# Kernel tuning notes

Measured on AMD Instinct MI355X. Metric: run time of the kernel, lower is better.

## Reference

```python
import jax, jax.numpy as jnp
import numpy as np

NUM_HEADS = 12
SCRA_SCALING = 10.0
EPS = 1e-12  # F.normalize default eps


def setup_inputs() -> dict:
    key = jax.random.key(0)
    ks = jax.random.split(key, 5)
    B, N, C = 2, 2048, 768
    return {
        "x": jax.random.normal(ks[0], (B, N, C), dtype=jnp.float32),
        "qkv_w": jax.random.normal(ks[1], (3 * C, C), dtype=jnp.float32) * 0.02,
        "qkv_b": jax.random.normal(ks[2], (3 * C,), dtype=jnp.float32) * 0.02,
        "proj_w": jax.random.normal(ks[3], (C, C), dtype=jnp.float32) * 0.02,
        "proj_b": jax.random.normal(ks[4], (C,), dtype=jnp.float32) * 0.02,
    }


def reference(x, qkv_w, qkv_b, proj_w, proj_b):
    B, N, C = x.shape
    H = NUM_HEADS
    D = C // H
    scale = D ** -0.5

    xt = jnp.transpose(x, (1, 0, 2))  # [N, B, C]
    qkv = xt @ qkv_w.T + qkv_b        # [N, B, 3C]
    q, k, v = jnp.split(qkv, 3, axis=-1)

    def to_bh(t):  # [N, B, C] -> [B*H, N, D]
        return jnp.transpose(t.reshape(N, B * H, D), (1, 0, 2))

    q, k, v = to_bh(q), to_bh(k), to_bh(v)

    # Stage 1: standard attention
    attn = jax.nn.softmax(jnp.einsum('bnd,bmd->bnm', q, k) * scale, axis=-1)
    out = jnp.einsum('bnm,bmd->bnd', attn, v)  # [B*H, N, D]
    out = jnp.transpose(out, (1, 0, 2)).reshape(N, B, C)
    out = out @ proj_w.T + proj_b              # first proj
    out = jnp.transpose(out.reshape(N, B * H, D), (1, 0, 2))  # [B*H, N, D]

    # Stage 2: self-correlation attention with data-dependent masking
    norm = jnp.linalg.norm(out, axis=-1, keepdims=True)
    sim_tokens = out / jnp.maximum(norm, EPS)
    sim = jnp.einsum('bnd,bmd->bnm', sim_tokens, sim_tokens) * SCRA_SCALING
    sim = jnp.where(sim < 0, -jnp.inf, sim)
    sim = jax.nn.softmax(sim, axis=-1)
    out2 = jnp.einsum('bnm,bmd->bnd', sim, v)
    out2 = jnp.transpose(out2, (1, 0, 2)).reshape(N, B, C)
    out2 = out2 @ proj_w.T + proj_b            # second proj (same weights)

    return jnp.transpose(out2, (1, 0, 2))      # [B, N, C]
```

## Files before the change

kernel.cpp:

```cpp
#include <hip/hip_runtime.h>

typedef unsigned short u16;
typedef __bf16 bf16_t;
typedef bf16_t bf16x8 __attribute__((ext_vector_type(8)));
typedef float f32x4 __attribute__((ext_vector_type(4)));

static __device__ __forceinline__ u16 f2bf(float f) {
  unsigned u = __builtin_bit_cast(unsigned, f);
  u += 0x7FFFu + ((u >> 16) & 1u);
  return (u16)(u >> 16);
}
static __device__ __forceinline__ bf16x8 ldfrag(const u16* p) {
  return __builtin_bit_cast(bf16x8, *(const uint4*)p);
}
static __device__ __forceinline__ float fexp2(float x) {
#if __has_builtin(__builtin_amdgcn_exp2f)
  return __builtin_amdgcn_exp2f(x);
#else
  return __expf(x * 0.69314718056f);
#endif
}
static __device__ __forceinline__ unsigned pack_hi16(unsigned hi, unsigned lo) {
#if __has_builtin(__builtin_amdgcn_perm)
  return __builtin_amdgcn_perm(hi, lo, 0x07060302u);
#else
  return (lo >> 16) | (hi & 0xFFFF0000u);
#endif
}
static __device__ __forceinline__ int sw(int row, int chunk) {
  return (row << 6) + ((chunk ^ (row & 7)) << 3);
}

#define XSZ 3145728
#define QWSZ 1769472
#define PWSZ 589824

__global__ __launch_bounds__(256) void convert_all(
    const float* __restrict__ x, const float* __restrict__ qw,
    const float* __restrict__ pw, u16* __restrict__ xb,
    u16* __restrict__ qwb, u16* __restrict__ pwb)
{
  const int i = (blockIdx.x * 256 + threadIdx.x) * 8;
  const float* src; u16* dst; int off;
  if (i < XSZ) { src = x; dst = xb; off = i; }
  else if (i < XSZ + QWSZ) { src = qw; dst = qwb; off = i - XSZ; }
  else { src = pw; dst = pwb; off = i - (XSZ + QWSZ); }
  float4 a = *(const float4*)(src + off), b = *(const float4*)(src + off + 4);
  u16 t[8] = {f2bf(a.x), f2bf(a.y), f2bf(a.z), f2bf(a.w),
              f2bf(b.x), f2bf(b.y), f2bf(b.z), f2bf(b.w)};
  *(uint4*)(dst + off) = *(const uint4*)t;
}

template<int MODE>
__global__ __launch_bounds__(256, 3) void gemm_nt(
    const u16* __restrict__ A, const u16* __restrict__ W,
    const float* __restrict__ bias,
    u16* __restrict__ d0, u16* __restrict__ d1, u16* __restrict__ d2,
    float* __restrict__ df)
{
  __shared__ __align__(16) u16 sA[2][64 * 64];
  __shared__ __align__(16) u16 sB[2][128 * 64];
  const int tid = threadIdx.x;
  const int m0 = blockIdx.y * 64, n0 = blockIdx.x * 128;
  const int w = tid >> 6, lane = tid & 63, l16 = lane & 15, quad = lane >> 4;
  const int wm = (w >> 1) * 32, wn = (w & 1) * 64;

  f32x4 acc[2][4] = {};
  const int sr = tid >> 3, ch = tid & 7, sc = ch * 8;

  #pragma unroll
  for (int p = 0; p < 2; p++)
    *(uint4*)(sA[0] + sw(sr + p * 32, ch)) =
        *(const uint4*)(A + (size_t)(m0 + sr + p * 32) * 768 + sc);
  #pragma unroll
  for (int p = 0; p < 4; p++)
    *(uint4*)(sB[0] + sw(sr + p * 32, ch)) =
        *(const uint4*)(W + (size_t)(n0 + sr + p * 32) * 768 + sc);
  __syncthreads();

  for (int kt = 0; kt < 12; kt++) {
    const int buf = kt & 1;
    const bool pre = (kt + 1 < 12);
    uint4 rab[2], rb[4];
    if (pre) {
      const int kc = (kt + 1) * 64 + sc;
      #pragma unroll
      for (int p = 0; p < 2; p++)
        rab[p] = *(const uint4*)(A + (size_t)(m0 + sr + p * 32) * 768 + kc);
      #pragma unroll
      for (int p = 0; p < 4; p++)
        rb[p] = *(const uint4*)(W + (size_t)(n0 + sr + p * 32) * 768 + kc);
    }
    #pragma unroll
    for (int ks = 0; ks < 2; ks++) {
      bf16x8 af[2], bfv[4];
      #pragma unroll
      for (int i = 0; i < 2; i++)
        af[i] = ldfrag(sA[buf] + sw(wm + i * 16 + l16, ks * 4 + quad));
      #pragma unroll
      for (int i = 0; i < 4; i++)
        bfv[i] = ldfrag(sB[buf] + sw(wn + i * 16 + l16, ks * 4 + quad));
      #pragma unroll
      for (int mi = 0; mi < 2; mi++)
        #pragma unroll
        for (int ni = 0; ni < 4; ni++)
          acc[mi][ni] = __builtin_amdgcn_mfma_f32_16x16x32_bf16(af[mi], bfv[ni], acc[mi][ni], 0, 0, 0);
    }
    if (pre) {
      #pragma unroll
      for (int p = 0; p < 2; p++)
        *(uint4*)(sA[buf ^ 1] + sw(sr + p * 32, ch)) = rab[p];
      #pragma unroll
      for (int p = 0; p < 4; p++)
        *(uint4*)(sB[buf ^ 1] + sw(sr + p * 32, ch)) = rb[p];
    }
    __syncthreads();
  }

  if (MODE == 0) {
    #pragma unroll
    for (int ni = 0; ni < 4; ni++) {
      const int gn = n0 + wn + ni * 16 + l16;
      const float bv = bias[gn];
      const int which = gn / 768;
      const int c = gn - which * 768, hh = c >> 6, d = c & 63;
      #pragma unroll
      for (int mi = 0; mi < 2; mi++) {
        const int gm0 = m0 + wm + mi * 16 + quad * 4;
        const int bb = gm0 >> 11, nt0 = gm0 & 2047;
        if (which == 2) {
          u16 t[4];
          #pragma unroll
          for (int r = 0; r < 4; r++) t[r] = f2bf(acc[mi][ni][r] + bv);
          *(uint2*)(d2 + (((size_t)(bb * 12 + hh)) * 64 + d) * 2048 + nt0) =
              *(const uint2*)t;
        } else {
          u16* dst = (which == 0) ? d0 : d1;
          #pragma unroll
          for (int r = 0; r < 4; r++)
            dst[(((size_t)(bb * 12 + hh)) * 2048 + nt0 + r) * 64 + d] =
                f2bf(acc[mi][ni][r] + bv);
        }
      }
    }
  } else if (MODE == 1) {
    #pragma unroll
    for (int mi = 0; mi < 2; mi++) {
      #pragma unroll
      for (int r = 0; r < 4; r++) {
        float v[4]; float ss = 0.f;
        #pragma unroll
        for (int ni = 0; ni < 4; ni++) {
          v[ni] = acc[mi][ni][r] + bias[n0 + wn + ni * 16 + l16];
          ss += v[ni] * v[ni];
        }
        #pragma unroll
        for (int off = 1; off < 16; off <<= 1) ss += __shfl_xor(ss, off);
        const float scl = 1.f / fmaxf(sqrtf(ss), 1e-12f);
        const int gm = m0 + wm + mi * 16 + quad * 4 + r;
        const int nt = gm >> 1, b = gm & 1;
        #pragma unroll
        for (int ni = 0; ni < 4; ni++) {
          const int gn = n0 + wn + ni * 16 + l16, h = gn >> 6, d = gn & 63;
          d0[(((size_t)(b * 12 + h)) * 2048 + nt) * 64 + d] = f2bf(v[ni] * scl);
        }
      }
    }
  } else {
    #pragma unroll
    for (int ni = 0; ni < 4; ni++) {
      const int gn = n0 + wn + ni * 16 + l16;
      const float bv = bias[gn];
      #pragma unroll
      for (int mi = 0; mi < 2; mi++) {
        #pragma unroll
        for (int r = 0; r < 4; r++) {
          const int gm = m0 + wm + mi * 16 + quad * 4 + r;
          const int nt = gm >> 1, b = gm & 1;
          df[((size_t)b * 2048 + nt) * 768 + gn] = acc[mi][ni][r] + bv;
        }
      }
    }
  }
}

template<int MODE>
__global__ __launch_bounds__(256, 2) void flash_attn(
    const u16* __restrict__ Qm, const u16* __restrict__ Km,
    const u16* __restrict__ VT,
    float* __restrict__ partN, float* __restrict__ partL)
{
  constexpr int N = 2048;
  __shared__ __align__(16) u16 sU[128 * 64];
  __shared__ __align__(16) u16 sK[64 * 64];
  __shared__ __align__(16) u16 sVT[64 * 64];
  const int tid = threadIdx.x;
  const int bh = blockIdx.y;
  const int qt = blockIdx.x >> 1, half = blockIdx.x & 1;
  const int m0 = qt * 128, j0 = half * 1024;
  const int w = tid >> 6, lane = tid & 63, l16 = lane & 15, quad = lane >> 4;

  constexpr float SC = (MODE == 1) ? 0.18033688011112042f
                                   : 14.426950408889634f;
  constexpr float M0 = (MODE == 1) ? 24.f : 14.6f;

  const u16* kbase = Km + (size_t)bh * N * 64;
  const u16* vbase = VT + (size_t)bh * 64 * N;
  const int qr = tid >> 1, qc = (tid & 1) * 4;
  const int sr4 = tid >> 2, c4 = tid & 3;
  {
    const u16* qp = Qm + ((size_t)bh * N + m0 + qr) * 64 + qc * 8;
    #pragma unroll
    for (int j = 0; j < 4; j++)
      *(uint4*)(sU + sw(qr, qc + j)) = *(const uint4*)(qp + j * 8);
    const u16* kp = kbase + (size_t)(j0 + sr4) * 64;
    *(uint4*)(sK + sw(sr4, c4))     = *(const uint4*)(kp + c4 * 8);
    *(uint4*)(sK + sw(sr4, c4 + 4)) = *(const uint4*)(kp + c4 * 8 + 32);
    const u16* vp = vbase + (size_t)sr4 * N + j0;
    *(uint4*)(sVT + sw(sr4, c4))     = *(const uint4*)(vp + c4 * 8);
    *(uint4*)(sVT + sw(sr4, c4 + 4)) = *(const uint4*)(vp + c4 * 8 + 32);
  }
  __syncthreads();
  bf16x8 qf[2][2];
  #pragma unroll
  for (int qg = 0; qg < 2; qg++) {
    qf[qg][0] = ldfrag(sU + sw(w * 32 + qg * 16 + l16, quad));
    qf[qg][1] = ldfrag(sU + sw(w * 32 + qg * 16 + l16, quad + 4));
  }
  asm volatile("s_waitcnt lgkmcnt(0)" ::: "memory");

  bf16x8 ones;
  #pragma unroll
  for (int i = 0; i < 8; i++) ones[i] = (bf16_t)1.0f;

  f32x4 oacc[2][4] = {};
  f32x4 lacc[2] = {};

  for (int it = 0; it < 16; it++) {
    uint4 pk0, pk1, pv0, pv1;
    const bool pre = (it + 1 < 16);
    if (pre) {
      const int j1 = j0 + (it + 1) * 64;
      const u16* kp = kbase + (size_t)(j1 + sr4) * 64;
      pk0 = *(const uint4*)(kp + c4 * 8);
      pk1 = *(const uint4*)(kp + c4 * 8 + 32);
      const u16* vp = vbase + (size_t)sr4 * N + j1;
      pv0 = *(const uint4*)(vp + c4 * 8);
      pv1 = *(const uint4*)(vp + c4 * 8 + 32);
    }

    f32x4 s[2][4];
    #pragma unroll
    for (int jt = 0; jt < 4; jt++) {
      bf16x8 kf0 = ldfrag(sK + sw(jt * 16 + l16, quad));
      bf16x8 kf1 = ldfrag(sK + sw(jt * 16 + l16, quad + 4));
      #pragma unroll
      for (int qg = 0; qg < 2; qg++) {
        f32x4 a = {};
        a = __builtin_amdgcn_mfma_f32_16x16x32_bf16(kf0, qf[qg][0], a, 0, 0, 0);
        a = __builtin_amdgcn_mfma_f32_16x16x32_bf16(kf1, qf[qg][1], a, 0, 0, 0);
        s[qg][jt] = a;
      }
    }

    #pragma unroll
    for (int qg = 0; qg < 2; qg++) {
      const int prow = w * 32 + qg * 16 + l16;
      #pragma unroll
      for (int jt = 0; jt < 4; jt++) {
        unsigned pu[4];
        #pragma unroll
        for (int r = 0; r < 4; r++) {
          const float a = s[qg][jt][r];
          float p = fexp2(fmaf(a, SC, -M0));
          if (MODE == 2 && a < 0.f) p = 0.f;
          pu[r] = __builtin_bit_cast(unsigned, p) & 0xFFFF0000u;
        }
        uint2 pkk;
        pkk.x = pack_hi16(pu[1], pu[0]);
        pkk.y = pack_hi16(pu[3], pu[2]);
        *(uint2*)(sU + sw(prow, 2 * jt + (quad >> 1)) + (quad & 1) * 4) = pkk;
      }
    }

    asm volatile("s_waitcnt lgkmcnt(0)" ::: "memory");
    bf16x8 pf[2][2];
    #pragma unroll
    for (int qg = 0; qg < 2; qg++) {
      pf[qg][0] = ldfrag(sU + sw(w * 32 + qg * 16 + l16, quad));
      pf[qg][1] = ldfrag(sU + sw(w * 32 + qg * 16 + l16, quad + 4));
    }

    #pragma unroll
    for (int d4 = 0; d4 < 4; d4++) {
      bf16x8 v0 = ldfrag(sVT + sw(d4 * 16 + l16, quad));
      bf16x8 v1 = ldfrag(sVT + sw(d4 * 16 + l16, quad + 4));
      #pragma unroll
      for (int qg = 0; qg < 2; qg++) {
        oacc[qg][d4] = __builtin_amdgcn_mfma_f32_16x16x32_bf16(v0, pf[qg][0], oacc[qg][d4], 0, 0, 0);
        oacc[qg][d4] = __builtin_amdgcn_mfma_f32_16x16x32_bf16(v1, pf[qg][1], oacc[qg][d4], 0, 0, 0);
      }
    }
    #pragma unroll
    for (int qg = 0; qg < 2; qg++) {
      lacc[qg] = __builtin_amdgcn_mfma_f32_16x16x32_bf16(ones, pf[qg][0], lacc[qg], 0, 0, 0);
      lacc[qg] = __builtin_amdgcn_mfma_f32_16x16x32_bf16(ones, pf[qg][1], lacc[qg], 0, 0, 0);
    }

    __syncthreads();
    if (pre) {
      *(uint4*)(sK + sw(sr4, c4))      = pk0;
      *(uint4*)(sK + sw(sr4, c4 + 4))  = pk1;
      *(uint4*)(sVT + sw(sr4, c4))     = pv0;
      *(uint4*)(sVT + sw(sr4, c4 + 4)) = pv1;
    }
    __syncthreads();
  }

  const int blk = bh * 32 + blockIdx.x;
  float* pN = partN + (size_t)blk * 8192 + tid * 32;
  #pragma unroll
  for (int qg = 0; qg < 2; qg++) {
    #pragma unroll
    for (int d4 = 0; d4 < 4; d4++)
      *(f32x4*)(pN + qg * 16 + d4 * 4) = oacc[qg][d4];
    if (quad == 0)
      partL[blk * 128 + w * 32 + qg * 16 + l16] = lacc[qg][0];
  }
}

__global__ __launch_bounds__(256) void combine_flash(
    const float* __restrict__ partN, const float* __restrict__ partL,
    u16* __restrict__ Ob)
{
  const int pair = blockIdx.x;
  const int bh = pair >> 4, qt = pair & 15;
  const int b = bh / 12, h = bh % 12;
  const int m0 = qt * 128;
  const int tid = threadIdx.x;
  const int w = tid >> 6, lane = tid & 63, l16 = lane & 15, quad = lane >> 4;
  const int blk0 = bh * 32 + qt * 2, blk1 = blk0 + 1;
  const float* n0 = partN + (size_t)blk0 * 8192 + tid * 32;
  const float* n1 = partN + (size_t)blk1 * 8192 + tid * 32;
  #pragma unroll
  for (int qg = 0; qg < 2; qg++) {
    const int qrow = w * 32 + qg * 16 + l16;
    const float l0 = partL[blk0 * 128 + qrow];
    const float l1 = partL[blk1 * 128 + qrow];
    const float inv = 1.f / fmaxf(l0 + l1, 1e-30f);
    const int query = m0 + qrow;
    u16* obase = Ob + ((size_t)query * 2 + b) * 768 + h * 64;
    #pragma unroll
    for (int d4 = 0; d4 < 4; d4++) {
      float4 a = *(const float4*)(n0 + qg * 16 + d4 * 4);
      float4 c = *(const float4*)(n1 + qg * 16 + d4 * 4);
      u16 t[4] = {f2bf((a.x + c.x) * inv), f2bf((a.y + c.y) * inv),
                  f2bf((a.z + c.z) * inv), f2bf((a.w + c.w) * inv)};
      *(uint2*)(obase + d4 * 16 + quad * 4) = *(const uint2*)t;
    }
  }
}

extern "C" void kernel_launch(void* const* d_in, const int* in_sizes, int n_in,
                              void* d_out, int out_size, void* d_ws, size_t ws_size,
                              hipStream_t stream) {
  const float* x      = (const float*)d_in[0];
  const float* qkv_w  = (const float*)d_in[1];
  const float* qkv_b  = (const float*)d_in[2];
  const float* proj_w = (const float*)d_in[3];
  const float* proj_b = (const float*)d_in[4];
  float* out = (float*)d_out;

  const size_t SZ = (size_t)24 * 2048 * 64;
  char* ws = (char*)d_ws;
  u16* vtb = (u16*)ws;
  size_t off = SZ * 2;
  u16* qwb = (u16*)(ws + off); off += (size_t)QWSZ * 2;
  u16* pwb = (u16*)(ws + off); off += (size_t)PWSZ * 2;
  u16* qb  = (u16*)(ws + off); off += SZ * 2;
  u16* kb  = (u16*)(ws + off); off += SZ * 2;
  float* partN = (float*)(ws + off); off += (size_t)768 * 8192 * 4;
  float* partL = (float*)(ws + off); off += (size_t)768 * 128 * 4;
  u16* xb = (u16*)partN;
  u16* o1 = qb;
  u16* o2 = qb;
  u16* st = kb;

  convert_all<<<2688, 256, 0, stream>>>(x, qkv_w, proj_w, xb, qwb, pwb);
  gemm_nt<0><<<dim3(18, 64), 256, 0, stream>>>(xb, qwb, qkv_b, qb, kb, vtb, nullptr);
  flash_attn<1><<<dim3(32, 24), 256, 0, stream>>>(qb, kb, vtb, partN, partL);
  combine_flash<<<384, 256, 0, stream>>>(partN, partL, o1);
  gemm_nt<1><<<dim3(6, 64), 256, 0, stream>>>(o1, pwb, proj_b, st, nullptr, nullptr, nullptr);
  flash_attn<2><<<dim3(32, 24), 256, 0, stream>>>(st, st, vtb, partN, partL);
  combine_flash<<<384, 256, 0, stream>>>(partN, partL, o2);
  gemm_nt<2><<<dim3(6, 64), 256, 0, stream>>>(o2, pwb, proj_b, nullptr, nullptr, nullptr, out);
}
```

Before: 231.9 us.

## Enlarge flash query tile to 256, split keys four ways, double-buffer K/V

The flash attention kernel now processes 256 query rows per block (64 per wave) and splits the key range into four 512-key chunks, so each K/V tile loaded into shared memory is reused across twice as many queries. K/V tiles are double-buffered in LDS, which removes one of the two block barriers per iteration, and the score-to-probability conversion is fused into the QK loop so the score array is no longer held. The combine kernel now sums four partials per query tile, and the workspace is rearranged so the qkv weight copy sits inside the enlarged partial buffer. In exchange, register pressure rises (twice as many accumulators per wave), LDS use grows, and the partial buffers written and read back are twice as large.

```diff
diff --git a/kernel.cpp b/kernel.cpp
--- a/kernel.cpp
+++ b/kernel.cpp
@@ -191,13 +191,13 @@
     float* __restrict__ partN, float* __restrict__ partL)
 {
   constexpr int N = 2048;
-  __shared__ __align__(16) u16 sU[128 * 64];
-  __shared__ __align__(16) u16 sK[64 * 64];
-  __shared__ __align__(16) u16 sVT[64 * 64];
+  __shared__ __align__(16) u16 sU[256 * 64];
+  __shared__ __align__(16) u16 sK[2][64 * 64];
+  __shared__ __align__(16) u16 sVT[2][64 * 64];
   const int tid = threadIdx.x;
   const int bh = blockIdx.y;
-  const int qt = blockIdx.x >> 1, half = blockIdx.x & 1;
-  const int m0 = qt * 128, j0 = half * 1024;
+  const int qt = blockIdx.x >> 2, quarter = blockIdx.x & 3;
+  const int m0 = qt * 256, j0 = quarter * 512;
   const int w = tid >> 6, lane = tid & 63, l16 = lane & 15, quad = lane >> 4;
 
   constexpr float SC = (MODE == 1) ? 0.18033688011112042f
@@ -206,26 +206,25 @@
 
   const u16* kbase = Km + (size_t)bh * N * 64;
   const u16* vbase = VT + (size_t)bh * 64 * N;
-  const int qr = tid >> 1, qc = (tid & 1) * 4;
   const int sr4 = tid >> 2, c4 = tid & 3;
   {
-    const u16* qp = Qm + ((size_t)bh * N + m0 + qr) * 64 + qc * 8;
-    #pragma unroll
-    for (int j = 0; j < 4; j++)
-      *(uint4*)(sU + sw(qr, qc + j)) = *(const uint4*)(qp + j * 8);
+    const u16* qp = Qm + ((size_t)bh * N + m0 + tid) * 64;
+    #pragma unroll
+    for (int j = 0; j < 8; j++)
+      *(uint4*)(sU + sw(tid, j)) = *(const uint4*)(qp + j * 8);
     const u16* kp = kbase + (size_t)(j0 + sr4) * 64;
-    *(uint4*)(sK + sw(sr4, c4))     = *(const uint4*)(kp + c4 * 8);
-    *(uint4*)(sK + sw(sr4, c4 + 4)) = *(const uint4*)(kp + c4 * 8 + 32);
+    *(uint4*)(sK[0] + sw(sr4, c4))     = *(const uint4*)(kp + c4 * 8);
+    *(uint4*)(sK[0] + sw(sr4, c4 + 4)) = *(const uint4*)(kp + c4 * 8 + 32);
     const u16* vp = vbase + (size_t)sr4 * N + j0;
-    *(uint4*)(sVT + sw(sr4, c4))     = *(const uint4*)(vp + c4 * 8);
-    *(uint4*)(sVT + sw(sr4, c4 + 4)) = *(const uint4*)(vp + c4 * 8 + 32);
+    *(uint4*)(sVT[0] + sw(sr4, c4))     = *(const uint4*)(vp + c4 * 8);
+    *(uint4*)(sVT[0] + sw(sr4, c4 + 4)) = *(const uint4*)(vp + c4 * 8 + 32);
   }
   __syncthreads();
-  bf16x8 qf[2][2];
-  #pragma unroll
-  for (int qg = 0; qg < 2; qg++) {
-    qf[qg][0] = ldfrag(sU + sw(w * 32 + qg * 16 + l16, quad));
-    qf[qg][1] = ldfrag(sU + sw(w * 32 + qg * 16 + l16, quad + 4));
+  bf16x8 qf[4][2];
+  #pragma unroll
+  for (int qg = 0; qg < 4; qg++) {
+    qf[qg][0] = ldfrag(sU + sw(w * 64 + qg * 16 + l16, quad));
+    qf[qg][1] = ldfrag(sU + sw(w * 64 + qg * 16 + l16, quad + 4));
   }
   asm volatile("s_waitcnt lgkmcnt(0)" ::: "memory");
 
@@ -233,12 +232,18 @@
   #pragma unroll
   for (int i = 0; i < 8; i++) ones[i] = (bf16_t)1.0f;
 
-  f32x4 oacc[2][4] = {};
-  f32x4 lacc[2] = {};
-
-  for (int it = 0; it < 16; it++) {
+  f32x4 oacc[4][4] = {};
+  f32x4 lacc[4] = {};
+
+  for (int it = 0; it < 8; it++) {
+    const int buf = it & 1;
+    const u16* sKb = sK[buf];
+    const u16* sVb = sVT[buf];
+    u16* sKn = sK[buf ^ 1];
+    u16* sVn = sVT[buf ^ 1];
+
     uint4 pk0, pk1, pv0, pv1;
-    const bool pre = (it + 1 < 16);
+    const bool pre = (it + 1 < 8);
     if (pre) {
       const int j1 = j0 + (it + 1) * 64;
       const u16* kp = kbase + (size_t)(j1 + sr4) * 64;
@@ -249,83 +254,72 @@
       pv1 = *(const uint4*)(vp + c4 * 8 + 32);
     }
 
-    f32x4 s[2][4];
     #pragma unroll
     for (int jt = 0; jt < 4; jt++) {
-      bf16x8 kf0 = ldfrag(sK + sw(jt * 16 + l16, quad));
-      bf16x8 kf1 = ldfrag(sK + sw(jt * 16 + l16, quad + 4));
-      #pragma unroll
-      for (int qg = 0; qg < 2; qg++) {
+      bf16x8 kf0 = ldfrag(sKb + sw(jt * 16 + l16, quad));
+      bf16x8 kf1 = ldfrag(sKb + sw(jt * 16 + l16, quad + 4));
+      #pragma unroll
+      for (int qg = 0; qg < 4; qg++) {
         f32x4 a = {};
         a = __builtin_amdgcn_mfma_f32_16x16x32_bf16(kf0, qf[qg][0], a, 0, 0, 0);
         a = __builtin_amdgcn_mfma_f32_16x16x32_bf16(kf1, qf[qg][1], a, 0, 0, 0);
-        s[qg][jt] = a;
-      }
-    }
-
-    #pragma unroll
-    for (int qg = 0; qg < 2; qg++) {
-      const int prow = w * 32 + qg * 16 + l16;
-      #pragma unroll
-      for (int jt = 0; jt < 4; jt++) {
         unsigned pu[4];
         #pragma unroll
         for (int r = 0; r < 4; r++) {
-          const float a = s[qg][jt][r];
-          float p = fexp2(fmaf(a, SC, -M0));
-          if (MODE == 2 && a < 0.f) p = 0.f;
+          float p = fexp2(fmaf(a[r], SC, -M0));
+          if (MODE == 2 && a[r] < 0.f) p = 0.f;
           pu[r] = __builtin_bit_cast(unsigned, p) & 0xFFFF0000u;
         }
         uint2 pkk;
         pkk.x = pack_hi16(pu[1], pu[0]);
         pkk.y = pack_hi16(pu[3], pu[2]);
+        const int prow = w * 64 + qg * 16 + l16;
         *(uint2*)(sU + sw(prow, 2 * jt + (quad >> 1)) + (quad & 1) * 4) = pkk;
       }
     }
 
     asm volatile("s_waitcnt lgkmcnt(0)" ::: "memory");
-    bf16x8 pf[2][2];
-    #pragma unroll
-    for (int qg = 0; qg < 2; qg++) {
-      pf[qg][0] = ldfrag(sU + sw(w * 32 + qg * 16 + l16, quad));
-      pf[qg][1] = ldfrag(sU + sw(w * 32 + qg * 16 + l16, quad + 4));
+    bf16x8 pf[4][2];
+    #pragma unroll
+    for (int qg = 0; qg < 4; qg++) {
+      pf[qg][0] = ldfrag(sU + sw(w * 64 + qg * 16 + l16, quad));
+      pf[qg][1] = ldfrag(sU + sw(w * 64 + qg * 16 + l16, quad + 4));
+    }
+
+    if (pre) {
+      *(uint4*)(sKn + sw(sr4, c4))     = pk0;
+      *(uint4*)(sKn + sw(sr4, c4 + 4)) = pk1;
+      *(uint4*)(sVn + sw(sr4, c4))     = pv0;
+      *(uint4*)(sVn + sw(sr4, c4 + 4)) = pv1;
     }
 
     #pragma unroll
     for (int d4 = 0; d4 < 4; d4++) {
-      bf16x8 v0 = ldfrag(sVT + sw(d4 * 16 + l16, quad));
-      bf16x8 v1 = ldfrag(sVT + sw(d4 * 16 + l16, quad + 4));
-      #pragma unroll
-      for (int qg = 0; qg < 2; qg++) {
+      bf16x8 v0 = ldfrag(sVb + sw(d4 * 16 + l16, quad));
+      bf16x8 v1 = ldfrag(sVb + sw(d4 * 16 + l16, quad + 4));
+      #pragma unroll
+      for (int qg = 0; qg < 4; qg++) {
         oacc[qg][d4] = __builtin_amdgcn_mfma_f32_16x16x32_bf16(v0, pf[qg][0], oacc[qg][d4], 0, 0, 0);
         oacc[qg][d4] = __builtin_amdgcn_mfma_f32_16x16x32_bf16(v1, pf[qg][1], oacc[qg][d4], 0, 0, 0);
       }
     }
     #pragma unroll
-    for (int qg = 0; qg < 2; qg++) {
+    for (int qg = 0; qg < 4; qg++) {
       lacc[qg] = __builtin_amdgcn_mfma_f32_16x16x32_bf16(ones, pf[qg][0], lacc[qg], 0, 0, 0);
       lacc[qg] = __builtin_amdgcn_mfma_f32_16x16x32_bf16(ones, pf[qg][1], lacc[qg], 0, 0, 0);
     }
-
     __syncthreads();
-    if (pre) {
-      *(uint4*)(sK + sw(sr4, c4))      = pk0;
-      *(uint4*)(sK + sw(sr4, c4 + 4))  = pk1;
-      *(uint4*)(sVT + sw(sr4, c4))     = pv0;
-      *(uint4*)(sVT + sw(sr4, c4 + 4)) = pv1;
-    }
-    __syncthreads();
   }
 
   const int blk = bh * 32 + blockIdx.x;
-  float* pN = partN + (size_t)blk * 8192 + tid * 32;
-  #pragma unroll
-  for (int qg = 0; qg < 2; qg++) {
+  float* pN = partN + (size_t)blk * 16384 + tid * 64;
+  #pragma unroll
+  for (int qg = 0; qg < 4; qg++) {
     #pragma unroll
     for (int d4 = 0; d4 < 4; d4++)
       *(f32x4*)(pN + qg * 16 + d4 * 4) = oacc[qg][d4];
     if (quad == 0)
-      partL[blk * 128 + w * 32 + qg * 16 + l16] = lacc[qg][0];
+      partL[blk * 256 + w * 64 + qg * 16 + l16] = lacc[qg][0];
   }
 }
 
@@ -333,29 +327,37 @@
     const float* __restrict__ partN, const float* __restrict__ partL,
     u16* __restrict__ Ob)
 {
-  const int pair = blockIdx.x;
-  const int bh = pair >> 4, qt = pair & 15;
+  const int bh = blockIdx.x >> 3, qt = blockIdx.x & 7;
   const int b = bh / 12, h = bh % 12;
-  const int m0 = qt * 128;
+  const int m0 = qt * 256;
   const int tid = threadIdx.x;
   const int w = tid >> 6, lane = tid & 63, l16 = lane & 15, quad = lane >> 4;
-  const int blk0 = bh * 32 + qt * 2, blk1 = blk0 + 1;
-  const float* n0 = partN + (size_t)blk0 * 8192 + tid * 32;
-  const float* n1 = partN + (size_t)blk1 * 8192 + tid * 32;
-  #pragma unroll
-  for (int qg = 0; qg < 2; qg++) {
-    const int qrow = w * 32 + qg * 16 + l16;
-    const float l0 = partL[blk0 * 128 + qrow];
-    const float l1 = partL[blk1 * 128 + qrow];
-    const float inv = 1.f / fmaxf(l0 + l1, 1e-30f);
+  const int blkbase = bh * 32 + qt * 4;
+  const float* n0 = partN + (size_t)(blkbase + 0) * 16384 + tid * 64;
+  const float* n1 = partN + (size_t)(blkbase + 1) * 16384 + tid * 64;
+  const float* n2 = partN + (size_t)(blkbase + 2) * 16384 + tid * 64;
+  const float* n3 = partN + (size_t)(blkbase + 3) * 16384 + tid * 64;
+  #pragma unroll
+  for (int qg = 0; qg < 4; qg++) {
+    const int qrow = w * 64 + qg * 16 + l16;
+    const float l = partL[(blkbase + 0) * 256 + qrow] +
+                    partL[(blkbase + 1) * 256 + qrow] +
+                    partL[(blkbase + 2) * 256 + qrow] +
+                    partL[(blkbase + 3) * 256 + qrow];
+    const float inv = 1.f / fmaxf(l, 1e-30f);
     const int query = m0 + qrow;
     u16* obase = Ob + ((size_t)query * 2 + b) * 768 + h * 64;
     #pragma unroll
     for (int d4 = 0; d4 < 4; d4++) {
-      float4 a = *(const float4*)(n0 + qg * 16 + d4 * 4);
-      float4 c = *(const float4*)(n1 + qg * 16 + d4 * 4);
-      u16 t[4] = {f2bf((a.x + c.x) * inv), f2bf((a.y + c.y) * inv),
-                  f2bf((a.z + c.z) * inv), f2bf((a.w + c.w) * inv)};
+      const int o = qg * 16 + d4 * 4;
+      float4 a = *(const float4*)(n0 + o);
+      float4 c = *(const float4*)(n1 + o);
+      float4 e = *(const float4*)(n2 + o);
+      float4 g = *(const float4*)(n3 + o);
+      u16 t[4] = {f2bf((a.x + c.x + e.x + g.x) * inv),
+                  f2bf((a.y + c.y + e.y + g.y) * inv),
+                  f2bf((a.z + c.z + e.z + g.z) * inv),
+                  f2bf((a.w + c.w + e.w + g.w) * inv)};
       *(uint2*)(obase + d4 * 16 + quad * 4) = *(const uint2*)t;
     }
   }
@@ -375,13 +377,13 @@
   char* ws = (char*)d_ws;
   u16* vtb = (u16*)ws;
   size_t off = SZ * 2;
-  u16* qwb = (u16*)(ws + off); off += (size_t)QWSZ * 2;
   u16* pwb = (u16*)(ws + off); off += (size_t)PWSZ * 2;
   u16* qb  = (u16*)(ws + off); off += SZ * 2;
   u16* kb  = (u16*)(ws + off); off += SZ * 2;
-  float* partN = (float*)(ws + off); off += (size_t)768 * 8192 * 4;
-  float* partL = (float*)(ws + off); off += (size_t)768 * 128 * 4;
-  u16* xb = (u16*)partN;
+  float* partN = (float*)(ws + off); off += (size_t)768 * 16384 * 4;
+  float* partL = (float*)(ws + off); off += (size_t)768 * 256 * 4;
+  u16* xb  = (u16*)partN;
+  u16* qwb = (u16*)partN + XSZ;
   u16* o1 = qb;
   u16* o2 = qb;
   u16* st = kb;
@@ -389,9 +391,9 @@
   convert_all<<<2688, 256, 0, stream>>>(x, qkv_w, proj_w, xb, qwb, pwb);
   gemm_nt<0><<<dim3(18, 64), 256, 0, stream>>>(xb, qwb, qkv_b, qb, kb, vtb, nullptr);
   flash_attn<1><<<dim3(32, 24), 256, 0, stream>>>(qb, kb, vtb, partN, partL);
-  combine_flash<<<384, 256, 0, stream>>>(partN, partL, o1);
+  combine_flash<<<192, 256, 0, stream>>>(partN, partL, o1);
   gemm_nt<1><<<dim3(6, 64), 256, 0, stream>>>(o1, pwb, proj_b, st, nullptr, nullptr, nullptr);
   flash_attn<2><<<dim3(32, 24), 256, 0, stream>>>(st, st, vtb, partN, partL);
-  combine_flash<<<384, 256, 0, stream>>>(partN, partL, o2);
+  combine_flash<<<192, 256, 0, stream>>>(partN, partL, o2);
   gemm_nt<2><<<dim3(6, 64), 256, 0, stream>>>(o2, pwb, proj_b, nullptr, nullptr, nullptr, out);
 }
```

After: 268.2 us. +15.6%, slower.
